# Kernel tuning notes

Measured on AMD Instinct MI355X. Metric: run time of the kernel, lower is better.

The kernel has to match this reference:

```python
import jax, jax.numpy as jnp
import numpy as np

H = 16
D_MODEL = 1024
D_K = D_MODEL // H


def setup_inputs() -> dict:
    key = jax.random.key(0)
    ks = jax.random.split(key, 11)
    B, S = 4, 2048
    scale = 1.0 / np.sqrt(D_MODEL)
    inp = {
        "query": jax.random.normal(ks[0], (B, S, D_MODEL), dtype=jnp.float32),
        "key": jax.random.normal(ks[1], (B, S, D_MODEL), dtype=jnp.float32),
        "value": jax.random.normal(ks[2], (B, S, D_MODEL), dtype=jnp.float32),
        "Wq": jax.random.normal(ks[3], (D_MODEL, D_MODEL), dtype=jnp.float32) * scale,
        "bq": jnp.zeros((D_MODEL,), dtype=jnp.float32),
        "Wk": jax.random.normal(ks[4], (D_MODEL, D_MODEL), dtype=jnp.float32) * scale,
        "bk": jnp.zeros((D_MODEL,), dtype=jnp.float32),
        "Wv": jax.random.normal(ks[5], (D_MODEL, D_MODEL), dtype=jnp.float32) * scale,
        "bv": jnp.zeros((D_MODEL,), dtype=jnp.float32),
        "Wo": jax.random.normal(ks[6], (D_MODEL, D_MODEL), dtype=jnp.float32) * scale,
        "bo": jnp.zeros((D_MODEL,), dtype=jnp.float32),
    }
    return inp


def reference(query, key, value, Wq, bq, Wk, bk, Wv, bv, Wo, bo):
    B, S, _ = query.shape

    def proj(x, W, b):
        # nn.Linear: x @ W.T + b, then split heads -> [B, H, S, D_K]
        y = jnp.einsum("bsd,ed->bse", x, W) + b
        return y.reshape(B, S, H, D_K).transpose(0, 2, 1, 3)

    q = proj(query, Wq, bq)
    k = proj(key, Wk, bk)
    v = proj(value, Wv, bv)

    scores = jnp.einsum("bhqd,bhkd->bhqk", q, k) / jnp.sqrt(jnp.float32(D_K))
    attn = jax.nn.softmax(scores, axis=-1)
    out = jnp.einsum("bhqk,bhkd->bhqd", attn, v)  # [B,H,S,D_K]
    out = out.transpose(0, 2, 1, 3).reshape(B, S, H * D_K)
    # final linear (dropout disabled in eval / deterministic reference)
    return jnp.einsum("bsd,ed->bse", out, Wo) + bo
```

## Files before the change

kernel.cpp:

```cpp
#include <hip/hip_runtime.h>
#include <stdint.h>

typedef __attribute__((ext_vector_type(8))) short short8;
typedef __attribute__((ext_vector_type(4))) float floatx4;

#define DEV __device__ __forceinline__

DEV unsigned short f2bf(float x) {
  unsigned u = __float_as_uint(x);
  u += 0x7fffu + ((u >> 16) & 1u);
  return (unsigned short)(u >> 16);
}

DEV unsigned pkbf(float hi, float lo) {
  return __builtin_amdgcn_perm(__float_as_uint(hi) + 0x8000u,
                               __float_as_uint(lo) + 0x8000u, 0x07060302u);
}

DEV void load_lds16(const unsigned short* g, unsigned short* l) {
  __builtin_amdgcn_global_load_lds(
      (const __attribute__((address_space(1))) void*)g,
      (__attribute__((address_space(3))) void*)l, 16, 0, 0);
}

DEV void lds_fence() { asm volatile("" ::: "memory"); }

#define ASM_VMCNT(n) asm volatile("s_waitcnt vmcnt(" #n ")" ::: "memory")
DEV void sched_fence() { __builtin_amdgcn_sched_barrier(0); }

__global__ void cvt_all(const float* __restrict__ Wq, const float* __restrict__ Wk,
                        const float* __restrict__ Wv, const float* __restrict__ Wo,
                        const float* __restrict__ Xq, const float* __restrict__ Xk,
                        const float* __restrict__ Xv,
                        unsigned short* __restrict__ Wb, unsigned short* __restrict__ XqB,
                        unsigned short* __restrict__ XkB, unsigned short* __restrict__ XvB) {
  int bid = blockIdx.x;
  const float* src;
  unsigned short* dst;
  int off;
  if (bid < 4096) {
    int sel = bid >> 10;
    src = sel == 0 ? Wq : sel == 1 ? Wk : sel == 2 ? Wv : Wo;
    dst = Wb + (size_t)sel * 1048576;
    off = bid & 1023;
  } else {
    bid -= 4096;
    int sel = bid >> 13;
    src = sel == 0 ? Xq : sel == 1 ? Xk : Xv;
    dst = sel == 0 ? XqB : sel == 1 ? XkB : XvB;
    off = bid & 8191;
  }
  int i = (off * 256 + threadIdx.x) * 4;
  float4 v = *(const float4*)(src + i);
  uint2 o;
  o.x = pkbf(v.y, v.x);
  o.y = pkbf(v.w, v.z);
  *(uint2*)(dst + i) = o;
}

#define SCQ (0.125f * 1.44269504089f)
__global__ __launch_bounds__(256, 3) void qkv_gemm(
    const unsigned short* __restrict__ XqB, const unsigned short* __restrict__ XkB,
    const unsigned short* __restrict__ XvB,
    const unsigned short* __restrict__ Wb,
    const float* __restrict__ bq, const float* __restrict__ bk, const float* __restrict__ bv,
    unsigned short* __restrict__ Qp, unsigned short* __restrict__ Kp,
    unsigned short* __restrict__ VTp) {
  __shared__ alignas(16) unsigned short Xs[3][128 * 32];
  __shared__ alignas(16) unsigned short Ws[3][128 * 32];
  const int z = blockIdx.z;
  const unsigned short* X = z == 0 ? XqB : z == 1 ? XkB : XvB;
  const unsigned short* W = Wb + (size_t)z * 1048576;
  const float* bias = z == 0 ? bq : z == 1 ? bk : bv;

  const int tid = threadIdx.x;
  const int lane = tid & 63, wave = tid >> 6;
  const int lcol = lane & 15, quad = lane >> 4;
  const int wo = blockIdx.x * 128;
  const int xo = blockIdx.y * 128;
  const int wm = (wave & 1) * 64;
  const int wn = (wave >> 1) * 64;

  floatx4 acc[4][4];
  for (int mi = 0; mi < 4; ++mi)
    for (int ni = 0; ni < 4; ++ni)
      for (int r = 0; r < 4; ++r) acc[mi][ni][r] = 0.f;

  auto stage = [&](int kt, int buf) {
    const int k0 = kt * 32;
    int c = tid;
    load_lds16(W + (size_t)(wo + (c >> 2)) * 1024 + k0 + (c & 3) * 8, Ws[buf] + c * 8);
    load_lds16(X + (size_t)(xo + (c >> 2)) * 1024 + k0 + (c & 3) * 8, Xs[buf] + c * 8);
    c = tid + 256;
    load_lds16(W + (size_t)(wo + (c >> 2)) * 1024 + k0 + (c & 3) * 8, Ws[buf] + c * 8);
    load_lds16(X + (size_t)(xo + (c >> 2)) * 1024 + k0 + (c & 3) * 8, Xs[buf] + c * 8);
  };

  stage(0, 0);
  stage(1, 1);
  int cur = 0;
  for (int kt = 0; kt < 32; ++kt) {
    sched_fence();
    ASM_VMCNT(4);
    __builtin_amdgcn_s_barrier();
    sched_fence();
    int nb = cur + 2; if (nb >= 3) nb -= 3;
    stage((kt + 2) & 31, nb);
    const unsigned short* Ab = (z < 2) ? Ws[cur] : Xs[cur];
    const unsigned short* Bb = (z < 2) ? Xs[cur] : Ws[cur];
    short8 af[4], bfr[4];
#pragma unroll
    for (int mi = 0; mi < 4; ++mi)
      af[mi] = *(const short8*)(Ab + (wm + mi * 16 + lcol) * 32 + quad * 8);
#pragma unroll
    for (int ni = 0; ni < 4; ++ni)
      bfr[ni] = *(const short8*)(Bb + (wn + ni * 16 + lcol) * 32 + quad * 8);
#pragma unroll
    for (int mi = 0; mi < 4; ++mi)
#pragma unroll
      for (int ni = 0; ni < 4; ++ni)
        acc[mi][ni] = __builtin_amdgcn_mfma_f32_16x16x32_bf16(af[mi], bfr[ni], acc[mi][ni], 0, 0, 0);
    cur = (cur == 2) ? 0 : cur + 1;
  }

  if (z < 2) {
    unsigned short* Out = z == 0 ? Qp : Kp;
    const float scl = z == 0 ? SCQ : 1.f;
#pragma unroll
    for (int mi = 0; mi < 4; ++mi) {
      int dbase = wo + wm + mi * 16 + quad * 4;
      float4 bv4 = *(const float4*)(bias + dbase);
      int h = dbase >> 6, dk = dbase & 63;
#pragma unroll
      for (int ni = 0; ni < 4; ++ni) {
        int sg = xo + wn + ni * 16 + lcol;
        int bb = sg >> 11, ss = sg & 2047;
        uint2 o;
        o.x = pkbf((acc[mi][ni][1] + bv4.y) * scl, (acc[mi][ni][0] + bv4.x) * scl);
        o.y = pkbf((acc[mi][ni][3] + bv4.w) * scl, (acc[mi][ni][2] + bv4.z) * scl);
        *(uint2*)(Out + ((size_t)(bb * 16 + h) * 2048 + ss) * 64 + dk) = o;
      }
    }
  } else {
#pragma unroll
    for (int ni = 0; ni < 4; ++ni) {
      int dg = wo + wn + ni * 16 + lcol;
      float bvx = bias[dg];
      int h = dg >> 6, dk = dg & 63;
#pragma unroll
      for (int mi = 0; mi < 4; ++mi) {
        int sbase = xo + wm + mi * 16 + quad * 4;
        int bb = sbase >> 11, ss = sbase & 2047;
        uint2 o;
        o.x = pkbf(acc[mi][ni][1] + bvx, acc[mi][ni][0] + bvx);
        o.y = pkbf(acc[mi][ni][3] + bvx, acc[mi][ni][2] + bvx);
        *(uint2*)(VTp + ((size_t)(bb * 16 + h) * 64 + dk) * 2048 + ss) = o;
      }
    }
  }
}

__global__ __launch_bounds__(256, 3) void gemm_o(
    const unsigned short* __restrict__ A, const unsigned short* __restrict__ Bw,
    const float* __restrict__ bias, float* __restrict__ Out) {
  __shared__ alignas(16) unsigned short Cs[3][128 * 32];
  __shared__ alignas(16) unsigned short Wos[3][128 * 32];
  const int tid = threadIdx.x;
  const int lane = tid & 63, wave = tid >> 6;
  const int lcol = lane & 15, quad = lane >> 4;
  const int co = blockIdx.x * 128;
  const int so = blockIdx.y * 128;
  const int wm = (wave & 1) * 64;
  const int wn = (wave >> 1) * 64;

  floatx4 acc[4][4];
  for (int mi = 0; mi < 4; ++mi)
    for (int ni = 0; ni < 4; ++ni)
      for (int r = 0; r < 4; ++r) acc[mi][ni][r] = 0.f;

  auto stage = [&](int kt, int buf) {
    const int k0 = kt * 32;
    int c = tid;
    load_lds16(Bw + (size_t)(co + (c >> 2)) * 1024 + k0 + (c & 3) * 8, Wos[buf] + c * 8);
    load_lds16(A  + (size_t)(so + (c >> 2)) * 1024 + k0 + (c & 3) * 8, Cs[buf] + c * 8);
    c = tid + 256;
    load_lds16(Bw + (size_t)(co + (c >> 2)) * 1024 + k0 + (c & 3) * 8, Wos[buf] + c * 8);
    load_lds16(A  + (size_t)(so + (c >> 2)) * 1024 + k0 + (c & 3) * 8, Cs[buf] + c * 8);
  };

  stage(0, 0);
  stage(1, 1);
  int cur = 0;
  for (int kt = 0; kt < 32; ++kt) {
    sched_fence();
    ASM_VMCNT(4);
    __builtin_amdgcn_s_barrier();
    sched_fence();
    int nb = cur + 2; if (nb >= 3) nb -= 3;
    stage((kt + 2) & 31, nb);
    short8 af[4], bfr[4];
#pragma unroll
    for (int mi = 0; mi < 4; ++mi)
      af[mi] = *(const short8*)(Wos[cur] + (wm + mi * 16 + lcol) * 32 + quad * 8);
#pragma unroll
    for (int ni = 0; ni < 4; ++ni)
      bfr[ni] = *(const short8*)(Cs[cur] + (wn + ni * 16 + lcol) * 32 + quad * 8);
#pragma unroll
    for (int mi = 0; mi < 4; ++mi)
#pragma unroll
      for (int ni = 0; ni < 4; ++ni)
        acc[mi][ni] = __builtin_amdgcn_mfma_f32_16x16x32_bf16(af[mi], bfr[ni], acc[mi][ni], 0, 0, 0);
    cur = (cur == 2) ? 0 : cur + 1;
  }
#pragma unroll
  for (int mi = 0; mi < 4; ++mi) {
    int cb = co + wm + mi * 16 + quad * 4;
    float4 bv4 = *(const float4*)(bias + cb);
#pragma unroll
    for (int ni = 0; ni < 4; ++ni) {
      int sg = so + wn + ni * 16 + lcol;
      float4 o;
      o.x = acc[mi][ni][0] + bv4.x;
      o.y = acc[mi][ni][1] + bv4.y;
      o.z = acc[mi][ni][2] + bv4.z;
      o.w = acc[mi][ni][3] + bv4.w;
      *(float4*)(Out + (size_t)sg * 1024 + cb) = o;
    }
  }
}

__global__ __launch_bounds__(256, 4) void attn_kernel(
    const unsigned short* __restrict__ Qp, const unsigned short* __restrict__ Kp,
    const unsigned short* __restrict__ VTp, unsigned short* __restrict__ Ctx) {
  __shared__ alignas(16) unsigned short Ks[2][64 * 64];
  __shared__ alignas(16) unsigned short Vt[64 * 64];
  __shared__ alignas(16) unsigned short Ps[128 * 64];

  const int tid = threadIdx.x;
  const int lane = tid & 63, wave = tid >> 6;
  const int lcol = lane & 15, quad = lane >> 4;
  const int wq = wave * 32;
  const int qt = blockIdx.x, h = blockIdx.y, b = blockIdx.z;
  const size_t bh = (size_t)(b * 16 + h) * 2048 * 64;
  const unsigned short* Qb = Qp + bh + (size_t)qt * 128 * 64;
  const unsigned short* Kb = Kp + bh;
  const unsigned short* VTb = VTp + (size_t)(b * 16 + h) * 64 * 2048;

#pragma unroll
  for (int i = 0; i < 4; ++i) {
    int p = tid + i * 256;
    int row = p >> 3, pj = p & 7;
    load_lds16(Qb + row * 64 + ((pj ^ (row & 7)) * 8), Ps + p * 8);
  }
#pragma unroll
  for (int i = 0; i < 2; ++i) {
    int p = tid + i * 256;
    int kr = p >> 3, kj = p & 7;
    load_lds16(Kb + kr * 64 + ((kj ^ (kr & 7)) * 8), Ks[0] + p * 8);
  }
  __syncthreads();

  short8 qf[2][2];
#pragma unroll
  for (int ni = 0; ni < 2; ++ni)
#pragma unroll
    for (int ks = 0; ks < 2; ++ks) {
      int row = wq + ni * 16 + lcol;
      qf[ni][ks] = *(const short8*)(Ps + row * 64 + (((ks * 4 + quad) ^ (row & 7)) * 8));
    }

  float M[2] = {-1e30f, -1e30f};
  float L[2] = {0.f, 0.f};
  floatx4 Oacc[2][4];
  for (int mi = 0; mi < 2; ++mi)
    for (int nd = 0; nd < 4; ++nd)
      for (int r = 0; r < 4; ++r) Oacc[mi][nd][r] = 0.f;

  for (int jt = 0; jt < 32; ++jt) {
    const int cur = jt & 1;
#pragma unroll
    for (int i = 0; i < 2; ++i) {
      int p = tid + i * 256;
      int vr = p >> 3, vj = p & 7;
      load_lds16(VTb + (size_t)vr * 2048 + jt * 64 + ((vj ^ (vr & 7)) * 8), Vt + p * 8);
    }
    const int jn = (jt + 1) & 31;
#pragma unroll
    for (int i = 0; i < 2; ++i) {
      int p = tid + i * 256;
      int kr = p >> 3, kj = p & 7;
      load_lds16(Kb + (size_t)jn * 4096 + kr * 64 + ((kj ^ (kr & 7)) * 8), Ks[cur ^ 1] + p * 8);
    }

    const unsigned short* Kc = Ks[cur];
    floatx4 sacc[4][2];
    for (int mi = 0; mi < 4; ++mi)
      for (int ni = 0; ni < 2; ++ni)
        for (int r = 0; r < 4; ++r) sacc[mi][ni][r] = 0.f;
#pragma unroll
    for (int mi = 0; mi < 4; ++mi) {
      int row = mi * 16 + lcol;
      int sw = (row & 7);
      short8 kf0 = *(const short8*)(Kc + row * 64 + ((quad ^ sw) * 8));
      short8 kf1 = *(const short8*)(Kc + row * 64 + (((4 + quad) ^ sw) * 8));
#pragma unroll
      for (int ni = 0; ni < 2; ++ni) {
        sacc[mi][ni] = __builtin_amdgcn_mfma_f32_16x16x32_bf16(kf0, qf[ni][0], sacc[mi][ni], 0, 0, 0);
        sacc[mi][ni] = __builtin_amdgcn_mfma_f32_16x16x32_bf16(kf1, qf[ni][1], sacc[mi][ni], 0, 0, 0);
      }
    }

    float mx[2];
#pragma unroll
    for (int ni = 0; ni < 2; ++ni) {
      float pm[4];
#pragma unroll
      for (int mi = 0; mi < 4; ++mi)
        pm[mi] = fmaxf(fmaxf(sacc[mi][ni][0], sacc[mi][ni][1]),
                       fmaxf(sacc[mi][ni][2], sacc[mi][ni][3]));
      float m = fmaxf(fmaxf(pm[0], pm[1]), fmaxf(pm[2], pm[3]));
      m = fmaxf(m, __shfl_xor(m, 16));
      m = fmaxf(m, __shfl_xor(m, 32));
      mx[ni] = m;
    }
    const int skip = __all((mx[0] <= M[0] + 8.f) & (mx[1] <= M[1] + 8.f));
    float alpha[2] = {1.f, 1.f};
    if (!skip) {
#pragma unroll
      for (int ni = 0; ni < 2; ++ni) {
        float mnew = fmaxf(M[ni], mx[ni]);
        alpha[ni] = exp2f(M[ni] - mnew);
        M[ni] = mnew;
      }
#pragma unroll
      for (int mi = 0; mi < 2; ++mi)
#pragma unroll
        for (int r = 0; r < 4; ++r) {
          float a = __shfl(alpha[mi], quad * 4 + r);
          floatx4 av = {a, a, a, a};
#pragma unroll
          for (int nd = 0; nd < 4; ++nd) Oacc[mi][nd] *= av;
        }
    }
#pragma unroll
    for (int ni = 0; ni < 2; ++ni) {
      floatx4 mv = {M[ni], M[ni], M[ni], M[ni]};
      floatx4 rv = {0.f, 0.f, 0.f, 0.f};
#pragma unroll
      for (int mi = 0; mi < 4; ++mi) {
        floatx4 t = sacc[mi][ni] - mv;
        floatx4 p;
        p[0] = exp2f(t[0]); p[1] = exp2f(t[1]); p[2] = exp2f(t[2]); p[3] = exp2f(t[3]);
        sacc[mi][ni] = p;
        rv += p;
      }
      float rs = (rv[0] + rv[1]) + (rv[2] + rv[3]);
      rs += __shfl_xor(rs, 16);
      rs += __shfl_xor(rs, 32);
      L[ni] = skip ? (L[ni] + rs) : (L[ni] * alpha[ni] + rs);
    }

#pragma unroll
    for (int ni = 0; ni < 2; ++ni) {
      int q = wq + ni * 16 + lcol;
      int sw = q & 7;
#pragma unroll
      for (int mi = 0; mi < 4; ++mi) {
        uint2 pw;
        pw.x = pkbf(sacc[mi][ni][1], sacc[mi][ni][0]);
        pw.y = pkbf(sacc[mi][ni][3], sacc[mi][ni][2]);
        int j = 2 * mi + (quad >> 1);
        *(uint2*)(Ps + q * 64 + ((j ^ sw) * 8) + (quad & 1) * 4) = pw;
      }
    }
    lds_fence();

    sched_fence();
    ASM_VMCNT(2);
    __builtin_amdgcn_s_barrier();
    sched_fence();

#pragma unroll
    for (int kk = 0; kk < 2; ++kk) {
      short8 pf[2];
#pragma unroll
      for (int mi = 0; mi < 2; ++mi) {
        int q = wq + mi * 16 + lcol;
        pf[mi] = *(const short8*)(Ps + q * 64 + (((kk * 4 + quad) ^ (q & 7)) * 8));
      }
#pragma unroll
      for (int nd = 0; nd < 4; ++nd) {
        int d = nd * 16 + lcol;
        short8 vf = *(const short8*)(Vt + d * 64 + (((kk * 4 + quad) ^ (d & 7)) * 8));
#pragma unroll
        for (int mi = 0; mi < 2; ++mi)
          Oacc[mi][nd] = __builtin_amdgcn_mfma_f32_16x16x32_bf16(pf[mi], vf, Oacc[mi][nd], 0, 0, 0);
      }
    }
    lds_fence();
    __syncthreads();
  }

  float linv[2] = {1.f / L[0], 1.f / L[1]};
#pragma unroll
  for (int mi = 0; mi < 2; ++mi)
#pragma unroll
    for (int r = 0; r < 4; ++r) {
      float li = __shfl(linv[mi], quad * 4 + r);
      int q = wq + mi * 16 + quad * 4 + r;
      int sw = q & 7;
#pragma unroll
      for (int nd = 0; nd < 4; ++nd) {
        int j = 2 * nd + (lcol >> 3);
        Ps[q * 64 + ((j ^ sw) * 8) + (lcol & 7)] = f2bf(Oacc[mi][nd][r] * li);
      }
    }
  __syncthreads();
#pragma unroll
  for (int i = 0; i < 4; ++i) {
    int c = tid + i * 256;
    int row = c >> 3, pj = c & 7;
    uint4 v = *(const uint4*)(Ps + row * 64 + ((pj ^ (row & 7)) * 8));
    *(uint4*)(Ctx + ((size_t)(b * 2048 + qt * 128 + row)) * 1024 + h * 64 + pj * 8) = v;
  }
}

extern "C" void kernel_launch(void* const* d_in, const int* in_sizes, int n_in,
                              void* d_out, int out_size, void* d_ws, size_t ws_size,
                              hipStream_t stream) {
  const float* query = (const float*)d_in[0];
  const float* key_  = (const float*)d_in[1];
  const float* value = (const float*)d_in[2];
  const float* Wq = (const float*)d_in[3];
  const float* bq = (const float*)d_in[4];
  const float* Wk = (const float*)d_in[5];
  const float* bk = (const float*)d_in[6];
  const float* Wv = (const float*)d_in[7];
  const float* bv = (const float*)d_in[8];
  const float* Wo = (const float*)d_in[9];
  const float* bo = (const float*)d_in[10];

  char* w = (char*)d_ws;
  unsigned short* Wb  = (unsigned short*)w; w += (size_t)4 * 1024 * 1024 * 2;
  unsigned short* Qp  = (unsigned short*)w; w += (size_t)8192 * 1024 * 2;
  unsigned short* Kp  = (unsigned short*)w; w += (size_t)8192 * 1024 * 2;
  unsigned short* VTp = (unsigned short*)w; w += (size_t)8192 * 1024 * 2;
  unsigned short* Ctx = (unsigned short*)w; w += (size_t)8192 * 1024 * 2;

  unsigned short* XqB = (unsigned short*)d_out;
  unsigned short* XkB = (unsigned short*)d_out + (size_t)8192 * 1024;
  unsigned short* XvB = Ctx;

  cvt_all<<<28672, 256, 0, stream>>>(Wq, Wk, Wv, Wo, query, key_, value,
                                     Wb, XqB, XkB, XvB);

  qkv_gemm<<<dim3(8, 64, 3), 256, 0, stream>>>(XqB, XkB, XvB, Wb,
                                               bq, bk, bv, Qp, Kp, VTp);

  attn_kernel<<<dim3(16, 16, 4), 256, 0, stream>>>(Qp, Kp, VTp, Ctx);

  gemm_o<<<dim3(8, 64), 256, 0, stream>>>(Ctx, Wb + (size_t)3 * 1048576, bo, (float*)d_out);
}
```

Measured before the change: 400.8 us.

## Remap blocks for XCD locality and compute softmax row sums via MFMA

Block indices in both GEMMs and in the attention kernel are remapped so that blocks sharing K/V heads or weight tiles land on the same XCD, which should improve L2 reuse. The softmax denominator is now accumulated by an extra MFMA against a ones vector, using the bf16-rounded P. This removes the per-tile exp-sum reductions and cross-lane shuffles, and the max shuffles now run only when a rescale is needed. Packing to bf16 uses the hardware v_cvt_pk_bf16_f32 instruction instead of the perm-based rounding. The cost is a few extra MFMAs and accumulator registers per tile.

```diff
diff --git a/kernel.cpp b/kernel.cpp
--- a/kernel.cpp
+++ b/kernel.cpp
@@ -15,6 +15,12 @@
 DEV unsigned pkbf(float hi, float lo) {
   return __builtin_amdgcn_perm(__float_as_uint(hi) + 0x8000u,
                                __float_as_uint(lo) + 0x8000u, 0x07060302u);
+}
+
+DEV unsigned cvtpk(float a, float b) {
+  unsigned r;
+  asm("v_cvt_pk_bf16_f32 %0, %1, %2" : "=v"(r) : "v"(a), "v"(b));
+  return r;
 }
 
 DEV void load_lds16(const unsigned short* g, unsigned short* l) {
@@ -76,8 +82,10 @@
   const int tid = threadIdx.x;
   const int lane = tid & 63, wave = tid >> 6;
   const int lcol = lane & 15, quad = lane >> 4;
-  const int wo = blockIdx.x * 128;
-  const int xo = blockIdx.y * 128;
+  const int n2 = blockIdx.x + 8 * blockIdx.y;
+  const int xcd = n2 & 7, ii = n2 >> 3;
+  const int wo = (ii >> 3) * 128;
+  const int xo = (xcd * 8 + (ii & 7)) * 128;
   const int wm = (wave & 1) * 64;
   const int wn = (wave >> 1) * 64;
 
@@ -168,8 +176,10 @@
   const int tid = threadIdx.x;
   const int lane = tid & 63, wave = tid >> 6;
   const int lcol = lane & 15, quad = lane >> 4;
-  const int co = blockIdx.x * 128;
-  const int so = blockIdx.y * 128;
+  const int n2 = blockIdx.x + 8 * blockIdx.y;
+  const int xcd = n2 & 7, ii = n2 >> 3;
+  const int co = (ii >> 3) * 128;
+  const int so = (xcd * 8 + (ii & 7)) * 128;
   const int wm = (wave & 1) * 64;
   const int wn = (wave >> 1) * 64;
 
@@ -240,11 +250,15 @@
   const int lane = tid & 63, wave = tid >> 6;
   const int lcol = lane & 15, quad = lane >> 4;
   const int wq = wave * 32;
-  const int qt = blockIdx.x, h = blockIdx.y, b = blockIdx.z;
-  const size_t bh = (size_t)(b * 16 + h) * 2048 * 64;
+  const int n = blockIdx.x + 16 * (blockIdx.y + 16 * blockIdx.z);
+  const int xcd = n & 7, ii = n >> 3;
+  const int hb = xcd * 8 + (ii & 7);
+  const int qt = ii >> 3;
+  const size_t bh = (size_t)hb * 2048 * 64;
+  const int b = hb >> 4;
   const unsigned short* Qb = Qp + bh + (size_t)qt * 128 * 64;
   const unsigned short* Kb = Kp + bh;
-  const unsigned short* VTb = VTp + (size_t)(b * 16 + h) * 64 * 2048;
+  const unsigned short* VTb = VTp + bh;
 
 #pragma unroll
   for (int i = 0; i < 4; ++i) {
@@ -269,12 +283,18 @@
       qf[ni][ks] = *(const short8*)(Ps + row * 64 + (((ks * 4 + quad) ^ (row & 7)) * 8));
     }
 
+  short8 ones;
+#pragma unroll
+  for (int j = 0; j < 8; ++j) ones[j] = (short)0x3f80;
+
   float M[2] = {-1e30f, -1e30f};
-  float L[2] = {0.f, 0.f};
   floatx4 Oacc[2][4];
-  for (int mi = 0; mi < 2; ++mi)
+  floatx4 OaccL[2];
+  for (int mi = 0; mi < 2; ++mi) {
     for (int nd = 0; nd < 4; ++nd)
       for (int r = 0; r < 4; ++r) Oacc[mi][nd][r] = 0.f;
+    for (int r = 0; r < 4; ++r) OaccL[mi][r] = 0.f;
+  }
 
   for (int jt = 0; jt < 32; ++jt) {
     const int cur = jt & 1;
@@ -310,25 +330,27 @@
       }
     }
 
-    float mx[2];
+    float lmax[2];
 #pragma unroll
     for (int ni = 0; ni < 2; ++ni) {
-      float pm[4];
-#pragma unroll
-      for (int mi = 0; mi < 4; ++mi)
-        pm[mi] = fmaxf(fmaxf(sacc[mi][ni][0], sacc[mi][ni][1]),
-                       fmaxf(sacc[mi][ni][2], sacc[mi][ni][3]));
-      float m = fmaxf(fmaxf(pm[0], pm[1]), fmaxf(pm[2], pm[3]));
-      m = fmaxf(m, __shfl_xor(m, 16));
-      m = fmaxf(m, __shfl_xor(m, 32));
-      mx[ni] = m;
-    }
-    const int skip = __all((mx[0] <= M[0] + 8.f) & (mx[1] <= M[1] + 8.f));
-    float alpha[2] = {1.f, 1.f};
+      float a0 = fmaxf(fmaxf(sacc[0][ni][0], sacc[0][ni][1]), sacc[0][ni][2]);
+      float a1 = fmaxf(fmaxf(sacc[0][ni][3], sacc[1][ni][0]), sacc[1][ni][1]);
+      float a2 = fmaxf(fmaxf(sacc[1][ni][2], sacc[1][ni][3]), sacc[2][ni][0]);
+      float a3 = fmaxf(fmaxf(sacc[2][ni][1], sacc[2][ni][2]), sacc[2][ni][3]);
+      float a4 = fmaxf(fmaxf(sacc[3][ni][0], sacc[3][ni][1]), sacc[3][ni][2]);
+      float b0 = fmaxf(fmaxf(a0, a1), a2);
+      float b1 = fmaxf(fmaxf(a3, a4), sacc[3][ni][3]);
+      lmax[ni] = fmaxf(b0, b1);
+    }
+    const int skip = __all((lmax[0] <= M[0] + 8.f) & (lmax[1] <= M[1] + 8.f));
     if (!skip) {
+      float alpha[2];
 #pragma unroll
       for (int ni = 0; ni < 2; ++ni) {
-        float mnew = fmaxf(M[ni], mx[ni]);
+        float m = lmax[ni];
+        m = fmaxf(m, __shfl_xor(m, 16));
+        m = fmaxf(m, __shfl_xor(m, 32));
+        float mnew = fmaxf(M[ni], m);
         alpha[ni] = exp2f(M[ni] - mnew);
         M[ni] = mnew;
       }
@@ -340,24 +362,20 @@
           floatx4 av = {a, a, a, a};
 #pragma unroll
           for (int nd = 0; nd < 4; ++nd) Oacc[mi][nd] *= av;
+          OaccL[mi][r] *= a;
         }
     }
 #pragma unroll
     for (int ni = 0; ni < 2; ++ni) {
       floatx4 mv = {M[ni], M[ni], M[ni], M[ni]};
-      floatx4 rv = {0.f, 0.f, 0.f, 0.f};
 #pragma unroll
       for (int mi = 0; mi < 4; ++mi) {
         floatx4 t = sacc[mi][ni] - mv;
-        floatx4 p;
-        p[0] = exp2f(t[0]); p[1] = exp2f(t[1]); p[2] = exp2f(t[2]); p[3] = exp2f(t[3]);
-        sacc[mi][ni] = p;
-        rv += p;
-      }
-      float rs = (rv[0] + rv[1]) + (rv[2] + rv[3]);
-      rs += __shfl_xor(rs, 16);
-      rs += __shfl_xor(rs, 32);
-      L[ni] = skip ? (L[ni] + rs) : (L[ni] * alpha[ni] + rs);
+        sacc[mi][ni][0] = exp2f(t[0]);
+        sacc[mi][ni][1] = exp2f(t[1]);
+        sacc[mi][ni][2] = exp2f(t[2]);
+        sacc[mi][ni][3] = exp2f(t[3]);
+      }
     }
 
 #pragma unroll
@@ -367,8 +385,8 @@
 #pragma unroll
       for (int mi = 0; mi < 4; ++mi) {
         uint2 pw;
-        pw.x = pkbf(sacc[mi][ni][1], sacc[mi][ni][0]);
-        pw.y = pkbf(sacc[mi][ni][3], sacc[mi][ni][2]);
+        pw.x = cvtpk(sacc[mi][ni][0], sacc[mi][ni][1]);
+        pw.y = cvtpk(sacc[mi][ni][2], sacc[mi][ni][3]);
         int j = 2 * mi + (quad >> 1);
         *(uint2*)(Ps + q * 64 + ((j ^ sw) * 8) + (quad & 1) * 4) = pw;
       }
@@ -396,17 +414,19 @@
         for (int mi = 0; mi < 2; ++mi)
           Oacc[mi][nd] = __builtin_amdgcn_mfma_f32_16x16x32_bf16(pf[mi], vf, Oacc[mi][nd], 0, 0, 0);
       }
+#pragma unroll
+      for (int mi = 0; mi < 2; ++mi)
+        OaccL[mi] = __builtin_amdgcn_mfma_f32_16x16x32_bf16(pf[mi], ones, OaccL[mi], 0, 0, 0);
     }
     lds_fence();
     __syncthreads();
   }
 
-  float linv[2] = {1.f / L[0], 1.f / L[1]};
 #pragma unroll
   for (int mi = 0; mi < 2; ++mi)
 #pragma unroll
     for (int r = 0; r < 4; ++r) {
-      float li = __shfl(linv[mi], quad * 4 + r);
+      float li = 1.f / OaccL[mi][r];
       int q = wq + mi * 16 + quad * 4 + r;
       int sw = q & 7;
 #pragma unroll
@@ -421,7 +441,7 @@
     int c = tid + i * 256;
     int row = c >> 3, pj = c & 7;
     uint4 v = *(const uint4*)(Ps + row * 64 + ((pj ^ (row & 7)) * 8));
-    *(uint4*)(Ctx + ((size_t)(b * 2048 + qt * 128 + row)) * 1024 + h * 64 + pj * 8) = v;
+    *(uint4*)(Ctx + ((size_t)(b * 2048 + qt * 128 + row)) * 1024 + (hb & 15) * 64 + pj * 8) = v;
   }
 }
 
```

Result: faster. 374.9 us (-6.5%).
